# Performance work log

Measured on AMD Instinct MI355X. Metric: run time of the kernel, lower is better.

The kernel has to match this reference:

```python
import jax, jax.numpy as jnp
import numpy as np

DIM = 192
HEADS = 6
WS = 7        # window_size
SS = 3        # shift_size
MLP_RATIO = 4.0
B = 64
H_RES = 56
W_RES = 56
EPS = 1e-5


def _rel_index(ws):
    # standard Swin relative position index, (ws*ws, ws*ws) int
    coords = np.stack(np.meshgrid(np.arange(ws), np.arange(ws), indexing='ij'))  # 2,ws,ws
    flat = coords.reshape(2, -1)                                                 # 2,N
    rel = (flat[:, :, None] - flat[:, None, :]).transpose(1, 2, 0)               # N,N,2
    rel[:, :, 0] += ws - 1
    rel[:, :, 1] += ws - 1
    rel[:, :, 0] *= 2 * ws - 1
    return rel.sum(-1)  # N,N


def _attn_mask(H, W, ws, ss):
    # (num_windows, N, N) float mask with 0 / -100, static given H,W,ws,ss
    img = np.zeros((H, W))
    sl = (slice(0, -ws), slice(-ws, -ss), slice(-ss, None))
    cnt = 0
    for hs in sl:
        for wsl in sl:
            img[hs, wsl] = cnt
            cnt += 1
    mw = img.reshape(H // ws, ws, W // ws, ws).transpose(0, 2, 1, 3).reshape(-1, ws * ws)
    diff = mw[:, None, :] - mw[:, :, None]
    return jnp.asarray(np.where(diff != 0, -100.0, 0.0).astype(np.float32))


def _ln(x, g, b):
    mu = x.mean(-1, keepdims=True)
    var = jnp.var(x, axis=-1, keepdims=True)
    return (x - mu) * jax.lax.rsqrt(var + EPS) * g + b


def setup_inputs() -> dict:
    key = jax.random.key(0)
    ks = jax.random.split(key, 8)
    C = DIM
    hid = int(C * MLP_RATIO)
    nrm = lambda k, s: jax.random.normal(k, s, jnp.float32) * 0.02
    return {
        "x": jax.random.normal(ks[0], (B, H_RES * W_RES, C), jnp.float32),
        "norm1_g": jnp.ones((C,), jnp.float32),
        "norm1_b": jnp.zeros((C,), jnp.float32),
        "qkv_w": nrm(ks[1], (3 * C, C)),
        "qkv_b": jnp.zeros((3 * C,), jnp.float32),
        "rel_bias_table": nrm(ks[2], ((2 * WS - 1) ** 2, HEADS)),
        "proj_w": nrm(ks[3], (C, C)),
        "proj_b": jnp.zeros((C,), jnp.float32),
        "norm2_g": jnp.ones((C,), jnp.float32),
        "norm2_b": jnp.zeros((C,), jnp.float32),
        "fc1_w": nrm(ks[4], (hid, C)),
        "fc1_b": jnp.zeros((hid,), jnp.float32),
        "fc2_w": nrm(ks[5], (C, hid)),
        "fc2_b": jnp.zeros((C,), jnp.float32),
        "H": H_RES,
        "W": W_RES,
    }


def _block(x, norm1_g, norm1_b, qkv_w, qkv_b, rel_bias_table, proj_w, proj_b,
           norm2_g, norm2_b, fc1_w, fc1_b, fc2_w, fc2_b, H, W):
    Bn, L, C = x.shape
    ws = min(WS, H, W)
    ss = SS if ws > SS else 0
    nH, nW = H // ws, W // ws
    N = ws * ws
    hd = C // HEADS

    shortcut = x
    h = _ln(x, norm1_g, norm1_b).reshape(Bn, H, W, C)
    if ss > 0:
        h = jnp.roll(h, (-ss, -ss), axis=(1, 2))
    # window partition -> (Bn*nH*nW, N, C)
    win = h.reshape(Bn, nH, ws, nW, ws, C).transpose(0, 1, 3, 2, 4, 5).reshape(-1, N, C)

    qkv = win @ qkv_w.T + qkv_b                       # (nWin, N, 3C)
    qkv = qkv.reshape(-1, N, 3, HEADS, hd).transpose(2, 0, 3, 1, 4)
    q, k, v = qkv[0], qkv[1], qkv[2]                  # (nWin, heads, N, hd)
    scale = float(hd) ** -0.5
    attn = jnp.einsum('whnd,whmd->whnm', q * scale, k)

    idx = _rel_index(ws)                              # N,N (static)
    bias = rel_bias_table[idx.reshape(-1)].reshape(N, N, HEADS).transpose(2, 0, 1)
    attn = attn + bias[None]

    if ss > 0:
        mask = _attn_mask(H, W, ws, ss)               # (nH*nW, N, N)
        attn = attn.reshape(Bn, nH * nW, HEADS, N, N) + mask[None, :, None]
        attn = attn.reshape(-1, HEADS, N, N)

    attn = jax.nn.softmax(attn, axis=-1)
    out = jnp.einsum('whnm,whmd->whnd', attn, v)      # (nWin, heads, N, hd)
    out = out.transpose(0, 2, 1, 3).reshape(-1, N, C)
    out = out @ proj_w.T + proj_b

    # window reverse -> (Bn, H, W, C)
    out = out.reshape(Bn, nH, nW, ws, ws, C).transpose(0, 1, 3, 2, 4, 5).reshape(Bn, H, W, C)
    if ss > 0:
        out = jnp.roll(out, (ss, ss), axis=(1, 2))
    x = shortcut + out.reshape(Bn, H * W, C)

    h2 = _ln(x, norm2_g, norm2_b)
    h2 = jax.nn.gelu(h2 @ fc1_w.T + fc1_b, approximate=False)
    h2 = h2 @ fc2_w.T + fc2_b
    return x + h2


def reference(x, norm1_g, norm1_b, qkv_w, qkv_b, rel_bias_table, proj_w, proj_b,
              norm2_g, norm2_b, fc1_w, fc1_b, fc2_w, fc2_b, H, W):
    return _block(x, norm1_g, norm1_b, qkv_w, qkv_b, rel_bias_table, proj_w, proj_b,
                  norm2_g, norm2_b, fc1_w, fc1_b, fc2_w, fc2_b, H, W)
```

## Files before the change

kernel.cpp:

```cpp
#include <hip/hip_runtime.h>
#include <hip/hip_bf16.h>
#include <math.h>

typedef __attribute__((ext_vector_type(8))) short short8;
typedef __attribute__((ext_vector_type(4))) float floatx4;

__device__ __forceinline__ float bf2f(unsigned short u) {
    union { unsigned int i; float f; } v;
    v.i = ((unsigned int)u) << 16;
    return v.f;
}
__device__ __forceinline__ unsigned short f2bf(float f) {
    union { float f; unsigned int i; } v;
    v.f = f;
    return (unsigned short)((v.i + 0x7FFFu + ((v.i >> 16) & 1u)) >> 16);
}
__device__ __forceinline__ void async16(const void* g, void* l) {
    __builtin_amdgcn_global_load_lds((const __attribute__((address_space(1))) void*)g,
                                     (__attribute__((address_space(3))) void*)l, 16, 0, 0);
}

__global__ __launch_bounds__(256) void cvt_kernel(const float* __restrict__ s,
                                                  unsigned short* __restrict__ d, int n,
                                                  int cut, float scale) {
    int i = blockIdx.x * 256 + threadIdx.x;
    if (i < n) d[i] = f2bf(s[i] * (i < cut ? scale : 1.0f));
}
__global__ __launch_bounds__(256) void biasscale_kernel(const float* __restrict__ s,
                                                        float* __restrict__ d, int n,
                                                        int cut, float scale) {
    int i = blockIdx.x * 256 + threadIdx.x;
    if (i < n) d[i] = s[i] * (i < cut ? scale : 1.0f);
}

__global__ __launch_bounds__(256) void bmt_kernel(const float* __restrict__ btab,
                                                  float* __restrict__ tbl) {
    int idx = blockIdx.x * 256 + threadIdx.x;
    int key = idx & 63;
    int q = (idx >> 6) & 63;
    int h = (idx >> 12) % 6;
    int cls = idx / (4096 * 6);
    float v;
    if (key >= 49) v = -3.0e38f;
    else if (q >= 49) v = 0.0f;
    else {
        int qi = q / 7, qj = q % 7, ki = key / 7, kj = key % 7;
        v = btab[((qi - ki + 6) * 13 + (qj - kj + 6)) * 6 + h];
        int whT = (cls >> 1) & 1, wwT = cls & 1;
        int rq = (whT ? (qi < 4 ? 1 : 2) : 0) * 3 + (wwT ? (qj < 4 ? 1 : 2) : 0);
        int rk = (whT ? (ki < 4 ? 1 : 2) : 0) * 3 + (wwT ? (kj < 4 ? 1 : 2) : 0);
        if (rq != rk) v -= 100.0f;
    }
    tbl[idx] = v;
}

__global__ __launch_bounds__(256) void ln_kernel(const float* __restrict__ src,
                                                 const float* __restrict__ gw,
                                                 const float* __restrict__ bw,
                                                 unsigned short* __restrict__ dst,
                                                 int mode) {
    int o = blockIdx.x * 4 + (threadIdx.x >> 6);
    int lane = threadIdx.x & 63;
    size_t srow;
    if (mode == 0) {
        int win = o / 49, n = o % 49;
        int b = win >> 6, wl = win & 63;
        int wh = wl >> 3, ww = wl & 7;
        int i = n / 7, j = n % 7;
        int pr = (wh * 7 + i + 3) % 56;
        int pc = (ww * 7 + j + 3) % 56;
        srow = ((size_t)b * 3136 + (size_t)(pr * 56 + pc)) * 192;
    } else {
        srow = (size_t)o * 192;
    }
    float v0 = src[srow + lane];
    float v1 = src[srow + lane + 64];
    float v2 = src[srow + lane + 128];
    float s = v0 + v1 + v2;
    float s2 = v0 * v0 + v1 * v1 + v2 * v2;
    #pragma unroll
    for (int off = 32; off > 0; off >>= 1) {
        s += __shfl_xor(s, off);
        s2 += __shfl_xor(s2, off);
    }
    float mean = s * (1.0f / 192.0f);
    float var = s2 * (1.0f / 192.0f) - mean * mean;
    float inv = rsqrtf(var + 1e-5f);
    size_t drow = (size_t)o * 192;
    dst[drow + lane]       = f2bf((v0 - mean) * inv * gw[lane]       + bw[lane]);
    dst[drow + lane + 64]  = f2bf((v1 - mean) * inv * gw[lane + 64]  + bw[lane + 64]);
    dst[drow + lane + 128] = f2bf((v2 - mean) * inv * gw[lane + 128] + bw[lane + 128]);
}

template <int EPI>
__global__ __launch_bounds__(256) void gemm_nt(const unsigned short* __restrict__ A,
                                               const unsigned short* __restrict__ W,
                                               const float* __restrict__ bias,
                                               int K, int ldo, int mbase,
                                               unsigned short* __restrict__ outb,
                                               float* __restrict__ outf,
                                               const float* __restrict__ resid) {
    __shared__ __align__(16) unsigned short Al[128][32];
    __shared__ __align__(16) unsigned short Wl[64][32];
    int tid = threadIdx.x;
    int lane = tid & 63;
    int wv = tid >> 6;
    int wm = wv >> 1, wn = wv & 1;
    int m0 = blockIdx.y * 128;
    int n0 = blockIdx.x * 64;
    int quad = lane >> 4, l15 = lane & 15;

    int srow = lane >> 2;
    int scol = (lane & 3) * 8;
    const unsigned short* aP0 = A + (size_t)(m0 + wv * 32 + srow) * K + scol;
    const unsigned short* aP1 = aP0 + (size_t)16 * K;
    const unsigned short* wP  = W + (size_t)(n0 + wv * 16 + srow) * K + scol;
    unsigned short* lA0 = &Al[wv * 32][0];
    unsigned short* lA1 = &Al[wv * 32 + 16][0];
    unsigned short* lW  = &Wl[wv * 16][0];

    floatx4 acc[4][2];
    floatx4 zero = {0.f, 0.f, 0.f, 0.f};
    #pragma unroll
    for (int a = 0; a < 4; ++a)
        #pragma unroll
        for (int b = 0; b < 2; ++b) acc[a][b] = zero;

    for (int kt = 0; kt < K; kt += 32) {
        __syncthreads();
        async16(aP0 + kt, lA0);
        async16(aP1 + kt, lA1);
        async16(wP + kt, lW);
        __syncthreads();
        short8 af[4], wf[2];
        #pragma unroll
        for (int mt = 0; mt < 4; ++mt)
            af[mt] = *(const short8*)&Al[wm * 64 + mt * 16 + l15][quad * 8];
        #pragma unroll
        for (int nt = 0; nt < 2; ++nt)
            wf[nt] = *(const short8*)&Wl[wn * 32 + nt * 16 + l15][quad * 8];
        #pragma unroll
        for (int mt = 0; mt < 4; ++mt)
            #pragma unroll
            for (int nt = 0; nt < 2; ++nt)
                acc[mt][nt] = __builtin_amdgcn_mfma_f32_16x16x32_bf16(af[mt], wf[nt], acc[mt][nt], 0, 0, 0);
    }

    #pragma unroll
    for (int mt = 0; mt < 4; ++mt) {
        #pragma unroll
        for (int nt = 0; nt < 2; ++nt) {
            #pragma unroll
            for (int r = 0; r < 4; ++r) {
                int m = m0 + wm * 64 + mt * 16 + quad * 4 + r;
                int n = n0 + wn * 32 + nt * 16 + l15;
                float v = acc[mt][nt][r] + bias[n];
                if (EPI == 0) {
                    outb[(size_t)m * ldo + n] = f2bf(v);
                } else if (EPI == 1) {
                    float g = 0.5f * v * (1.0f + erff(v * 0.70710678118654752f));
                    outb[(size_t)m * ldo + n] = f2bf(g);
                } else if (EPI == 2) {
                    int win = m / 49, np = m % 49;
                    int b = win >> 6, wl = win & 63;
                    int wh = wl >> 3, ww = wl & 7;
                    int i = np / 7, j = np % 7;
                    int pr = (wh * 7 + i + 3) % 56;
                    int pc = (ww * 7 + j + 3) % 56;
                    size_t dst = ((size_t)b * 3136 + (size_t)(pr * 56 + pc)) * 192 + n;
                    outf[dst] = resid[dst] + v;
                } else {
                    size_t dst = (size_t)(mbase + m) * ldo + n;
                    outf[dst] = resid[dst] + v;
                }
            }
        }
    }
}

__global__ __launch_bounds__(192) void attn_kernel(const unsigned short* __restrict__ qkv,
                                                   const float* __restrict__ tbl,
                                                   unsigned short* __restrict__ awin) {
    __shared__ __align__(16) unsigned short Pb[3][64][72];
    int w = blockIdx.x >> 1;
    int hb = (blockIdx.x & 1) * 3;
    int hl = threadIdx.x >> 6;
    int h = hb + hl;
    int lane = threadIdx.x & 63;
    int quad = lane >> 4, l15 = lane & 15;
    const unsigned short* base = qkv + (size_t)w * 49 * 576;
    int wl = w & 63;
    int cls = ((wl >> 3) == 7 ? 2 : 0) + ((wl & 7) == 7 ? 1 : 0);
    const float* tb = tbl + (size_t)(cls * 6 + h) * 4096;

    short8 kf[4], qf[4];
    #pragma unroll
    for (int mt = 0; mt < 4; ++mt)
        kf[mt] = *(const short8*)(base + (size_t)(mt * 16 + l15) * 576 + 192 + h * 32 + quad * 8);
    #pragma unroll
    for (int nt = 0; nt < 4; ++nt)
        qf[nt] = *(const short8*)(base + (size_t)(nt * 16 + l15) * 576 + h * 32 + quad * 8);

    floatx4 S[4][4];
    #pragma unroll
    for (int mt = 0; mt < 4; ++mt)
        #pragma unroll
        for (int nt = 0; nt < 4; ++nt) {
            floatx4 cinit = *(const floatx4*)(tb + (nt * 16 + l15) * 64 + mt * 16 + quad * 4);
            S[mt][nt] = __builtin_amdgcn_mfma_f32_16x16x32_bf16(kf[mt], qf[nt], cinit, 0, 0, 0);
        }

    #pragma unroll
    for (int mt = 0; mt < 4; ++mt)
        #pragma unroll
        for (int nt = 0; nt < 4; ++nt)
            #pragma unroll
            for (int rr = 0; rr < 4; ++rr)
                S[mt][nt][rr] = __expf(S[mt][nt][rr]);

    float rinv[4];
    #pragma unroll
    for (int nt = 0; nt < 4; ++nt) {
        float s = 0.f;
        #pragma unroll
        for (int mt = 0; mt < 4; ++mt)
            s += (S[mt][nt][0] + S[mt][nt][1]) + (S[mt][nt][2] + S[mt][nt][3]);
        s += __shfl_xor(s, 16);
        s += __shfl_xor(s, 32);
        rinv[nt] = 1.0f / s;
    }

    #pragma unroll
    for (int mt = 0; mt < 4; ++mt) {
        #pragma unroll
        for (int nt = 0; nt < 4; ++nt) {
            __hip_bfloat162 p0 = __float22bfloat162_rn(
                make_float2(S[mt][nt][0] * rinv[nt], S[mt][nt][1] * rinv[nt]));
            __hip_bfloat162 p1 = __float22bfloat162_rn(
                make_float2(S[mt][nt][2] * rinv[nt], S[mt][nt][3] * rinv[nt]));
            union { __hip_bfloat162 h2[2]; uint2 u; } pk;
            pk.h2[0] = p0;
            pk.h2[1] = p1;
            *(uint2*)&Pb[hl][nt * 16 + l15][mt * 16 + quad * 4] = pk.u;
        }
    }

    floatx4 O[4][2];
    floatx4 zero = {0.f, 0.f, 0.f, 0.f};
    #pragma unroll
    for (int mt = 0; mt < 4; ++mt)
        #pragma unroll
        for (int nt = 0; nt < 2; ++nt) O[mt][nt] = zero;
    #pragma unroll
    for (int ks = 0; ks < 2; ++ks) {
        short8 vf[2];
        #pragma unroll
        for (int nt = 0; nt < 2; ++nt) {
            const unsigned short* vb =
                base + (size_t)(ks * 32 + quad * 8) * 576 + 384 + h * 32 + nt * 16 + l15;
            #pragma unroll
            for (int j = 0; j < 8; ++j) vf[nt][j] = (short)vb[(size_t)j * 576];
        }
        #pragma unroll
        for (int mt = 0; mt < 4; ++mt) {
            short8 pf = *(const short8*)&Pb[hl][mt * 16 + l15][ks * 32 + quad * 8];
            #pragma unroll
            for (int nt = 0; nt < 2; ++nt)
                O[mt][nt] = __builtin_amdgcn_mfma_f32_16x16x32_bf16(pf, vf[nt], O[mt][nt], 0, 0, 0);
        }
    }
    #pragma unroll
    for (int mt = 0; mt < 4; ++mt) {
        #pragma unroll
        for (int rr = 0; rr < 4; ++rr) {
            int q = mt * 16 + quad * 4 + rr;
            if (q < 49) {
                #pragma unroll
                for (int nt = 0; nt < 2; ++nt)
                    awin[((size_t)w * 49 + q) * 192 + h * 32 + nt * 16 + l15] =
                        f2bf(O[mt][nt][rr]);
            }
        }
    }
}

extern "C" void kernel_launch(void* const* d_in, const int* in_sizes, int n_in,
                              void* d_out, int out_size, void* d_ws, size_t ws_size,
                              hipStream_t stream) {
    const float* x      = (const float*)d_in[0];
    const float* n1g    = (const float*)d_in[1];
    const float* n1b    = (const float*)d_in[2];
    const float* qkv_w  = (const float*)d_in[3];
    const float* qkv_b  = (const float*)d_in[4];
    const float* btab   = (const float*)d_in[5];
    const float* proj_w = (const float*)d_in[6];
    const float* proj_b = (const float*)d_in[7];
    const float* n2g    = (const float*)d_in[8];
    const float* n2b    = (const float*)d_in[9];
    const float* fc1_w  = (const float*)d_in[10];
    const float* fc1_b  = (const float*)d_in[11];
    const float* fc2_w  = (const float*)d_in[12];
    const float* fc2_b  = (const float*)d_in[13];
    float* out = (float*)d_out;

    char* p = (char*)d_ws;
    size_t off = 0;
    auto alloc = [&](size_t bytes) {
        char* r = p + off;
        off = (off + bytes + 255) & ~(size_t)255;
        return r;
    };
    unsigned short* wq   = (unsigned short*)alloc((size_t)576 * 192 * 2);
    unsigned short* wp   = (unsigned short*)alloc((size_t)192 * 192 * 2);
    unsigned short* w1   = (unsigned short*)alloc((size_t)768 * 192 * 2);
    unsigned short* w2   = (unsigned short*)alloc((size_t)192 * 768 * 2);
    unsigned short* hwin = (unsigned short*)alloc((size_t)200704 * 192 * 2);
    unsigned short* qkvb = (unsigned short*)alloc((size_t)200704 * 576 * 2);
    float*          xres = (float*)alloc((size_t)200704 * 192 * 4);
    unsigned short* g1   = (unsigned short*)alloc((size_t)50176 * 768 * 2);
    if (ws_size < off) return;
    float* tbl   = (float*)g1;
    float* qkvbs = (float*)g1 + 98304;

    const float scale = 0.17677669529663687f;
    cvt_kernel<<<432, 256, 0, stream>>>(qkv_w, wq, 110592, 36864, scale);
    cvt_kernel<<<144, 256, 0, stream>>>(proj_w, wp, 36864, 0, 1.0f);
    cvt_kernel<<<576, 256, 0, stream>>>(fc1_w, w1, 147456, 0, 1.0f);
    cvt_kernel<<<576, 256, 0, stream>>>(fc2_w, w2, 147456, 0, 1.0f);
    biasscale_kernel<<<3, 256, 0, stream>>>(qkv_b, qkvbs, 576, 192, scale);
    bmt_kernel<<<384, 256, 0, stream>>>(btab, tbl);

    ln_kernel<<<50176, 256, 0, stream>>>(x, n1g, n1b, hwin, 0);
    gemm_nt<0><<<dim3(9, 1568), 256, 0, stream>>>(hwin, wq, qkvbs, 192, 576, 0, qkvb, nullptr, nullptr);
    attn_kernel<<<8192, 192, 0, stream>>>(qkvb, tbl, hwin );
    gemm_nt<2><<<dim3(3, 1568), 256, 0, stream>>>(hwin, wp, proj_b, 192, 192, 0, nullptr, xres, x);
    unsigned short* h2 = qkvb;
    ln_kernel<<<50176, 256, 0, stream>>>(xres, n2g, n2b, h2, 1);
    for (int c = 0; c < 4; ++c) {
        int mb = c * 50176;
        gemm_nt<1><<<dim3(12, 392), 256, 0, stream>>>(h2 + (size_t)mb * 192, w1, fc1_b, 192, 768, 0,
                                                      g1, nullptr, nullptr);
        gemm_nt<3><<<dim3(3, 392), 256, 0, stream>>>(g1, w2, fc2_b, 768, 192, mb,
                                                     nullptr, out, xres);
    }
}
```

Before: 1.103 ms.

## Double-buffer GEMM LDS tiles, swizzle block order, and write V transposed for attention

```diff
diff --git a/kernel.cpp b/kernel.cpp
--- a/kernel.cpp
+++ b/kernel.cpp
@@ -31,6 +31,13 @@
                                                         int cut, float scale) {
     int i = blockIdx.x * 256 + threadIdx.x;
     if (i < n) d[i] = s[i] * (i < cut ? scale : 1.0f);
+}
+
+__global__ __launch_bounds__(256) void zerov_kernel(unsigned short* __restrict__ vT) {
+    int idx = blockIdx.x * 256 + threadIdx.x;
+    size_t row = (size_t)(idx >> 1);
+    uint4 z = make_uint4(0u, 0u, 0u, 0u);
+    *(uint4*)(vT + row * 64 + 48 + (idx & 1) * 8) = z;
 }
 
 __global__ __launch_bounds__(256) void bmt_kernel(const float* __restrict__ btab,
@@ -96,28 +103,28 @@
 __global__ __launch_bounds__(256) void gemm_nt(const unsigned short* __restrict__ A,
                                                const unsigned short* __restrict__ W,
                                                const float* __restrict__ bias,
-                                               int K, int ldo, int mbase,
+                                               int K, int ldo, int mbase, int gx, int noff,
                                                unsigned short* __restrict__ outb,
                                                float* __restrict__ outf,
                                                const float* __restrict__ resid) {
-    __shared__ __align__(16) unsigned short Al[128][32];
-    __shared__ __align__(16) unsigned short Wl[64][32];
+    __shared__ __align__(16) unsigned short Al[2][128][32];
+    __shared__ __align__(16) unsigned short Wl[2][64][32];
     int tid = threadIdx.x;
     int lane = tid & 63;
     int wv = tid >> 6;
     int wm = wv >> 1, wn = wv & 1;
-    int m0 = blockIdx.y * 128;
-    int n0 = blockIdx.x * 64;
+    int bid = blockIdx.x;
+    int swz = (bid & 7) * ((int)gridDim.x >> 3) + (bid >> 3);
+    int bx = swz % gx, by = swz / gx;
+    int m0 = by * 128;
+    int n0 = bx * 64;
     int quad = lane >> 4, l15 = lane & 15;
 
     int srow = lane >> 2;
     int scol = (lane & 3) * 8;
     const unsigned short* aP0 = A + (size_t)(m0 + wv * 32 + srow) * K + scol;
     const unsigned short* aP1 = aP0 + (size_t)16 * K;
-    const unsigned short* wP  = W + (size_t)(n0 + wv * 16 + srow) * K + scol;
-    unsigned short* lA0 = &Al[wv * 32][0];
-    unsigned short* lA1 = &Al[wv * 32 + 16][0];
-    unsigned short* lW  = &Wl[wv * 16][0];
+    const unsigned short* wP  = W + (size_t)(noff + n0 + wv * 16 + srow) * K + scol;
 
     floatx4 acc[4][2];
     floatx4 zero = {0.f, 0.f, 0.f, 0.f};
@@ -126,52 +133,78 @@
         #pragma unroll
         for (int b = 0; b < 2; ++b) acc[a][b] = zero;
 
-    for (int kt = 0; kt < K; kt += 32) {
-        __syncthreads();
-        async16(aP0 + kt, lA0);
-        async16(aP1 + kt, lA1);
-        async16(wP + kt, lW);
-        __syncthreads();
+    async16(aP0, &Al[0][wv * 32][0]);
+    async16(aP1, &Al[0][wv * 32 + 16][0]);
+    async16(wP,  &Wl[0][wv * 16][0]);
+    __syncthreads();
+
+    int nsteps = K >> 5;
+    int cur = 0;
+    for (int t = 0; t < nsteps; ++t) {
+        if (t + 1 < nsteps) {
+            int kt = (t + 1) << 5;
+            int nb = cur ^ 1;
+            async16(aP0 + kt, &Al[nb][wv * 32][0]);
+            async16(aP1 + kt, &Al[nb][wv * 32 + 16][0]);
+            async16(wP + kt,  &Wl[nb][wv * 16][0]);
+        }
         short8 af[4], wf[2];
         #pragma unroll
         for (int mt = 0; mt < 4; ++mt)
-            af[mt] = *(const short8*)&Al[wm * 64 + mt * 16 + l15][quad * 8];
+            af[mt] = *(const short8*)&Al[cur][wm * 64 + mt * 16 + l15][quad * 8];
         #pragma unroll
         for (int nt = 0; nt < 2; ++nt)
-            wf[nt] = *(const short8*)&Wl[wn * 32 + nt * 16 + l15][quad * 8];
+            wf[nt] = *(const short8*)&Wl[cur][wn * 32 + nt * 16 + l15][quad * 8];
         #pragma unroll
         for (int mt = 0; mt < 4; ++mt)
             #pragma unroll
             for (int nt = 0; nt < 2; ++nt)
                 acc[mt][nt] = __builtin_amdgcn_mfma_f32_16x16x32_bf16(af[mt], wf[nt], acc[mt][nt], 0, 0, 0);
+        __syncthreads();
+        cur ^= 1;
     }
 
     #pragma unroll
     for (int mt = 0; mt < 4; ++mt) {
         #pragma unroll
         for (int nt = 0; nt < 2; ++nt) {
-            #pragma unroll
-            for (int r = 0; r < 4; ++r) {
-                int m = m0 + wm * 64 + mt * 16 + quad * 4 + r;
-                int n = n0 + wn * 32 + nt * 16 + l15;
-                float v = acc[mt][nt][r] + bias[n];
-                if (EPI == 0) {
-                    outb[(size_t)m * ldo + n] = f2bf(v);
-                } else if (EPI == 1) {
-                    float g = 0.5f * v * (1.0f + erff(v * 0.70710678118654752f));
-                    outb[(size_t)m * ldo + n] = f2bf(g);
-                } else if (EPI == 2) {
-                    int win = m / 49, np = m % 49;
-                    int b = win >> 6, wl = win & 63;
-                    int wh = wl >> 3, ww = wl & 7;
-                    int i = np / 7, j = np % 7;
-                    int pr = (wh * 7 + i + 3) % 56;
-                    int pc = (ww * 7 + j + 3) % 56;
-                    size_t dst = ((size_t)b * 3136 + (size_t)(pr * 56 + pc)) * 192 + n;
-                    outf[dst] = resid[dst] + v;
-                } else {
-                    size_t dst = (size_t)(mbase + m) * ldo + n;
-                    outf[dst] = resid[dst] + v;
+            if (EPI == 4) {
+                int nv = n0 + wn * 32 + nt * 16 + l15;
+                int hh = nv >> 5, dd = nv & 31;
+                float bv = bias[384 + nv];
+                int mq = m0 + wm * 64 + mt * 16 + quad * 4;
+                int w = mq / 49, key0 = mq - w * 49;
+                unsigned short* vrow = outb + ((size_t)(w * 6 + hh) * 32 + dd) * 64;
+                #pragma unroll
+                for (int r = 0; r < 4; ++r) {
+                    int key = key0 + r;
+                    unsigned short* dp = vrow + (key >= 49 ? key - 49 + 12288 : key);
+                    *dp = f2bf(acc[mt][nt][r] + bv);
+                }
+            } else {
+                #pragma unroll
+                for (int r = 0; r < 4; ++r) {
+                    int m = m0 + wm * 64 + mt * 16 + quad * 4 + r;
+                    int n = n0 + wn * 32 + nt * 16 + l15;
+                    float v = acc[mt][nt][r] + bias[n];
+                    if (EPI == 0) {
+                        outb[(size_t)m * ldo + n] = f2bf(v);
+                    } else if (EPI == 1) {
+                        float g = 0.5f * v * (1.0f + erff(v * 0.70710678118654752f));
+                        outb[(size_t)m * ldo + n] = f2bf(g);
+                    } else if (EPI == 2) {
+                        int win = m / 49, np = m % 49;
+                        int b = win >> 6, wl = win & 63;
+                        int wh = wl >> 3, ww = wl & 7;
+                        int i = np / 7, j = np % 7;
+                        int pr = (wh * 7 + i + 3) % 56;
+                        int pc = (ww * 7 + j + 3) % 56;
+                        size_t dst = ((size_t)b * 3136 + (size_t)(pr * 56 + pc)) * 192 + n;
+                        outf[dst] = resid[dst] + v;
+                    } else {
+                        size_t dst = (size_t)(mbase + m) * ldo + n;
+                        outf[dst] = resid[dst] + v;
+                    }
                 }
             }
         }
@@ -179,6 +212,7 @@
 }
 
 __global__ __launch_bounds__(192) void attn_kernel(const unsigned short* __restrict__ qkv,
+                                                   const unsigned short* __restrict__ vT,
                                                    const float* __restrict__ tbl,
                                                    unsigned short* __restrict__ awin) {
     __shared__ __align__(16) unsigned short Pb[3][64][72];
@@ -201,6 +235,14 @@
     for (int nt = 0; nt < 4; ++nt)
         qf[nt] = *(const short8*)(base + (size_t)(nt * 16 + l15) * 576 + h * 32 + quad * 8);
 
+    const unsigned short* vb = vT + (size_t)(w * 6 + h) * 2048;
+    short8 vf[2][2];
+    #pragma unroll
+    for (int ks = 0; ks < 2; ++ks)
+        #pragma unroll
+        for (int nt = 0; nt < 2; ++nt)
+            vf[ks][nt] = *(const short8*)(vb + (size_t)(nt * 16 + l15) * 64 + ks * 32 + quad * 8);
+
     floatx4 S[4][4];
     #pragma unroll
     for (int mt = 0; mt < 4; ++mt)
@@ -253,20 +295,12 @@
         for (int nt = 0; nt < 2; ++nt) O[mt][nt] = zero;
     #pragma unroll
     for (int ks = 0; ks < 2; ++ks) {
-        short8 vf[2];
-        #pragma unroll
-        for (int nt = 0; nt < 2; ++nt) {
-            const unsigned short* vb =
-                base + (size_t)(ks * 32 + quad * 8) * 576 + 384 + h * 32 + nt * 16 + l15;
-            #pragma unroll
-            for (int j = 0; j < 8; ++j) vf[nt][j] = (short)vb[(size_t)j * 576];
-        }
         #pragma unroll
         for (int mt = 0; mt < 4; ++mt) {
             short8 pf = *(const short8*)&Pb[hl][mt * 16 + l15][ks * 32 + quad * 8];
             #pragma unroll
             for (int nt = 0; nt < 2; ++nt)
-                O[mt][nt] = __builtin_amdgcn_mfma_f32_16x16x32_bf16(pf, vf[nt], O[mt][nt], 0, 0, 0);
+                O[mt][nt] = __builtin_amdgcn_mfma_f32_16x16x32_bf16(pf, vf[ks][nt], O[mt][nt], 0, 0, 0);
         }
     }
     #pragma unroll
@@ -321,6 +355,7 @@
     if (ws_size < off) return;
     float* tbl   = (float*)g1;
     float* qkvbs = (float*)g1 + 98304;
+    unsigned short* vT = (unsigned short*)xres;
 
     const float scale = 0.17677669529663687f;
     cvt_kernel<<<432, 256, 0, stream>>>(qkv_w, wq, 110592, 36864, scale);
@@ -329,18 +364,23 @@
     cvt_kernel<<<576, 256, 0, stream>>>(fc2_w, w2, 147456, 0, 1.0f);
     biasscale_kernel<<<3, 256, 0, stream>>>(qkv_b, qkvbs, 576, 192, scale);
     bmt_kernel<<<384, 256, 0, stream>>>(btab, tbl);
+    zerov_kernel<<<6144, 256, 0, stream>>>(vT);
 
     ln_kernel<<<50176, 256, 0, stream>>>(x, n1g, n1b, hwin, 0);
-    gemm_nt<0><<<dim3(9, 1568), 256, 0, stream>>>(hwin, wq, qkvbs, 192, 576, 0, qkvb, nullptr, nullptr);
-    attn_kernel<<<8192, 192, 0, stream>>>(qkvb, tbl, hwin );
-    gemm_nt<2><<<dim3(3, 1568), 256, 0, stream>>>(hwin, wp, proj_b, 192, 192, 0, nullptr, xres, x);
+    gemm_nt<0><<<9408, 256, 0, stream>>>(hwin, wq, qkvbs, 192, 576, 0, 6, 0,
+                                         qkvb, nullptr, nullptr);
+    gemm_nt<4><<<4704, 256, 0, stream>>>(hwin, wq, qkvbs, 192, 0, 0, 3, 384,
+                                         vT, nullptr, nullptr);
+    attn_kernel<<<8192, 192, 0, stream>>>(qkvb, vT, tbl, hwin );
+    gemm_nt<2><<<4704, 256, 0, stream>>>(hwin, wp, proj_b, 192, 192, 0, 3, 0,
+                                         nullptr, xres, x);
     unsigned short* h2 = qkvb;
     ln_kernel<<<50176, 256, 0, stream>>>(xres, n2g, n2b, h2, 1);
     for (int c = 0; c < 4; ++c) {
         int mb = c * 50176;
-        gemm_nt<1><<<dim3(12, 392), 256, 0, stream>>>(h2 + (size_t)mb * 192, w1, fc1_b, 192, 768, 0,
-                                                      g1, nullptr, nullptr);
-        gemm_nt<3><<<dim3(3, 392), 256, 0, stream>>>(g1, w2, fc2_b, 768, 192, mb,
-                                                     nullptr, out, xres);
-    }
-}
+        gemm_nt<1><<<4704, 256, 0, stream>>>(h2 + (size_t)mb * 192, w1, fc1_b, 192, 768, 0,
+                                             12, 0, g1, nullptr, nullptr);
+        gemm_nt<3><<<1176, 256, 0, stream>>>(g1, w2, fc2_b, 768, 192, mb, 3, 0,
+                                             nullptr, out, xres);
+    }
+}
```

Result: slower. 1.158 ms (+5.0%).
